# Kernel optimization log

Hardware: AMD Instinct MI355X
Metric: run time of the kernel (lower is better)

The kernel has to match this reference:

```python
import jax, jax.numpy as jnp
import numpy as np
from jax import lax

B, N = 4096, 512          # batch, sequence length (input_dim = 2*N)
H1, H2 = 64, 256          # hidden sizes of the two stacked LSTMs
E = 20                    # embed dim
OUT = 2


def _lstm_step(x, h, c, Wih, Whh, b):
    # gates in PyTorch order: i, f, g, o
    g = x @ Wih.T + h @ Whh.T + b
    i, f, gg, o = jnp.split(g, 4, axis=-1)
    c_new = jax.nn.sigmoid(f) * c + jax.nn.sigmoid(i) * jnp.tanh(gg)
    h_new = jax.nn.sigmoid(o) * jnp.tanh(c_new)
    return h_new, c_new


def setup_inputs() -> dict:
    key = jax.random.key(0)
    ks = jax.random.split(key, 9)
    s = lambda fan_in: 1.0 / np.sqrt(fan_in)
    return {
        "x": jax.random.normal(ks[0], (B, 2 * N), dtype=jnp.float32),
        "W_embed": jax.random.uniform(ks[1], (E, 2), minval=-s(2), maxval=s(2), dtype=jnp.float32),
        "Wih1": jax.random.uniform(ks[2], (4 * H1, E), minval=-s(H1), maxval=s(H1), dtype=jnp.float32),
        "Whh1": jax.random.uniform(ks[3], (4 * H1, H1), minval=-s(H1), maxval=s(H1), dtype=jnp.float32),
        "b1": jax.random.uniform(ks[4], (4 * H1,), minval=-s(H1), maxval=s(H1), dtype=jnp.float32),
        "Wih2": jax.random.uniform(ks[5], (4 * H2, H1), minval=-s(H2), maxval=s(H2), dtype=jnp.float32),
        "Whh2": jax.random.uniform(ks[6], (4 * H2, H2), minval=-s(H2), maxval=s(H2), dtype=jnp.float32),
        "b2": jax.random.uniform(ks[7], (4 * H2,), minval=-s(H2), maxval=s(H2), dtype=jnp.float32),
        "Wout": jax.random.uniform(ks[8], (OUT, H2), minval=-s(H2), maxval=s(H2), dtype=jnp.float32),
        "bout": jnp.zeros((OUT,), dtype=jnp.float32),
    }


def reference(x, W_embed, Wih1, Whh1, b1, Wih2, Whh2, b2, Wout, bout):
    b = x.shape[0]
    tokens = x.reshape(b, -1, 2).transpose(1, 0, 2)         # (n, b, 2)
    embedded = jax.nn.relu(tokens @ W_embed.T)              # (n, b, 20)

    def step(carry, xt):
        h, c = carry
        h, c = _lstm_step(xt, h, c, Wih1, Whh1, b1)
        return (h, c), None

    h0 = jnp.zeros((b, H1), dtype=x.dtype)
    (h64, _), _ = lax.scan(step, (h0, h0), embedded)        # last hidden (b, 64)

    # second LSTM applied to the 2-D last-hidden as a single timestep
    hz = jnp.zeros((b, H2), dtype=x.dtype)
    h256, _ = _lstm_step(h64, hz, hz, Wih2, Whh2, b2)       # (b, 256)

    return h256 @ Wout.T + bout                             # (b, 2)
```

## Files before the change

kernel.cpp:

```cpp
#include <hip/hip_runtime.h>

typedef _Float16 f16x8 __attribute__((ext_vector_type(8)));
typedef float    f32x4 __attribute__((ext_vector_type(4)));

#define NSTEP 512
#define CHUNK 8
#define NCHUNK (NSTEP / CHUNK)
#define LOG2E     1.4426950408889634f
#define TWOLOG2E  2.8853900817779268f

__device__ __forceinline__ float exp2_(float v) { return __builtin_amdgcn_exp2f(v); }

__device__ __forceinline__ float lstm_act_(float gi, float gf, float gg, float go, float& c) {
    float eg = exp2_(gg);
    float ei = exp2_(gi);
    float ef = exp2_(gf);
    float eo = exp2_(go);
    float X  = (eg + 1.0f) * (1.0f + ei);
    float Y  = 1.0f + ef;
    float r  = __builtin_amdgcn_rcpf(X * Y);
    c = fmaf(r * X, c, (eg - 1.0f) * (r * Y));
    float ec = exp2_(fminf(c * TWOLOG2E, 30.0f));
    float r2 = __builtin_amdgcn_rcpf((ec + 1.0f) * (1.0f + eo));
    return (ec - 1.0f) * r2;
}
__device__ __forceinline__ float sig_(float v) {
    return __builtin_amdgcn_rcpf(1.0f + exp2_(-v * LOG2E));
}
__device__ __forceinline__ float tanh_(float v) {
    return 1.0f - 2.0f * __builtin_amdgcn_rcpf(exp2_(v * TWOLOG2E) + 1.0f);
}

__global__ __launch_bounds__(1024, 1) void lstm_mfma16_kernel(
    const float* __restrict__ x,     const float* __restrict__ Wemb,
    const float* __restrict__ Wih1,  const float* __restrict__ Whh1,
    const float* __restrict__ b1,    const float* __restrict__ Wih2,
    const float* __restrict__ b2,    const float* __restrict__ Wout,
    const float* __restrict__ bout,  float* __restrict__ out)
{
    __shared__ __align__(16) _Float16 P[2][2][4][16][8];
    __shared__ __align__(16) _Float16 Pe[CHUNK][4][16][8];
    __shared__ __align__(16) float h2tmp[16 * 64];
    __shared__ __align__(16) float h2s[256 * 16];
    __shared__ float part[64 * 16 * 2];

    const int t   = threadIdx.x;
    const int l   = t & 63;
    const int tau = t >> 6;
    const int m   = l & 15;
    const int q   = l >> 4;
    const int b0  = blockIdx.x * 16;

    f16x8 whh[2], whE;
    {
        const int g = m & 3;
        const float sc = (g == 2) ? TWOLOG2E : -LOG2E;
        const int n = g * 64 + 4 * tau + (m >> 2);
        #pragma unroll
        for (int c = 0; c < 2; ++c) {
            #pragma unroll
            for (int jj = 0; jj < 8; ++jj)
                whh[c][jj] = (_Float16)(Whh1[n * 64 + c * 32 + (q << 3) + jj] * sc);
        }
        #pragma unroll
        for (int jj = 0; jj < 8; ++jj) {
            int k = (q << 3) + jj;
            whE[jj] = (_Float16)((k < 20) ? Wih1[n * 20 + k] * sc : 0.0f);
        }
    }
    f32x4 bias4;
    #pragma unroll
    for (int r = 0; r < 4; ++r) {
        float sc = (r == 2) ? TWOLOG2E : -LOG2E;
        bias4[r] = b1[r * 64 + 4 * tau + q] * sc;
    }

    const int myu = 4 * tau + q;
    _Float16* hw0 = &P[0][myu >> 5][(myu >> 3) & 3][m][myu & 7];

    const float* xp[3]; _Float16* pe[3];
    float we0[3], we1[3];
    bool val[3];
    float2 xv[3];
    #pragma unroll
    for (int k = 0; k < 3; ++k) {
        int v  = t + 1024 * k;
        val[k] = (v < CHUNK * 320);
        int vv = val[k] ? v : 0;
        int d  = vv % 20, pr = vv / 20;
        int bb = pr & 15, s = pr >> 4;
        we0[k] = Wemb[2 * d];
        we1[k] = Wemb[2 * d + 1];
        pe[k]  = &Pe[s][d >> 3][bb][d & 7];
        xp[k]  = x + (size_t)(b0 + bb) * (2 * NSTEP) + 2 * s;
        xv[k]  = *(const float2*)xp[k];
    }

    ((_Float16*)P)[t] = (_Float16)0.0f;
    {
        _Float16* pz = (_Float16*)Pe;
        #pragma unroll
        for (int k = 0; k < 4; ++k) pz[t + 1024 * k] = (_Float16)0.0f;
    }
    __syncthreads();

    float cst = 0.0f;
    for (int ch = 0; ch < NCHUNK; ++ch) {
        #pragma unroll
        for (int k = 0; k < 3; ++k)
            if (val[k])
                *pe[k] = (_Float16)fmaxf(fmaf(xv[k].x, we0[k], xv[k].y * we1[k]), 0.0f);
        if (ch + 1 < NCHUNK) {
            #pragma unroll
            for (int k = 0; k < 3; ++k) { xp[k] += 16; xv[k] = *(const float2*)xp[k]; }
        }
        __syncthreads();

        f32x4 ax[CHUNK];
        #pragma unroll
        for (int j = 0; j < CHUNK; ++j) {
            f16x8 fe = *(const f16x8*)&Pe[j][q][m][0];
            ax[j] = __builtin_amdgcn_mfma_f32_16x16x32_f16(whE, fe, bias4, 0, 0, 0);
        }

        #pragma unroll
        for (int j = 0; j < CHUNK; ++j) {
            const int pr = j & 1;
            f16x8 f0 = *(const f16x8*)&P[pr][0][q][m][0];
            f16x8 f1 = *(const f16x8*)&P[pr][1][q][m][0];
            f32x4 a = __builtin_amdgcn_mfma_f32_16x16x32_f16(whh[0], f0, ax[j], 0, 0, 0);
            a = __builtin_amdgcn_mfma_f32_16x16x32_f16(whh[1], f1, a, 0, 0, 0);
            float hv = lstm_act_(a[0], a[1], a[2], a[3], cst);
            hw0[(pr ^ 1) * 1024] = (_Float16)hv;
            __syncthreads();
        }
    }

    {
        int b = t >> 6, k = t & 63;
        h2tmp[t] = (float)P[0][k >> 5][(k >> 3) & 3][b][k & 7];
    }
    __syncthreads();

    {
        const int u = t & 255;
        const int bh0 = (t >> 8) * 4;
        float acci[4], accg[4], acco[4];
        float bi2 = b2[u], bg2 = b2[512 + u], bo2 = b2[768 + u];
        #pragma unroll
        for (int b = 0; b < 4; ++b) { acci[b] = bi2; accg[b] = bg2; acco[b] = bo2; }
        for (int k4 = 0; k4 < 64; k4 += 4) {
            float4 wi = *(const float4*)&Wih2[(size_t)u * 64 + k4];
            float4 wg = *(const float4*)&Wih2[(size_t)(512 + u) * 64 + k4];
            float4 wo = *(const float4*)&Wih2[(size_t)(768 + u) * 64 + k4];
            #pragma unroll
            for (int b = 0; b < 4; ++b) {
                float4 hb = *(const float4*)&h2tmp[(bh0 + b) * 64 + k4];
                acci[b] += wi.x * hb.x + wi.y * hb.y + wi.z * hb.z + wi.w * hb.w;
                accg[b] += wg.x * hb.x + wg.y * hb.y + wg.z * hb.z + wg.w * hb.w;
                acco[b] += wo.x * hb.x + wo.y * hb.y + wo.z * hb.z + wo.w * hb.w;
            }
        }
        #pragma unroll
        for (int b = 0; b < 4; ++b) {
            float c2 = sig_(acci[b]) * tanh_(accg[b]);
            h2s[u * 16 + bh0 + b] = sig_(acco[b]) * tanh_(c2);
        }
    }
    __syncthreads();

    {
        int b = t & 15, grp = t >> 4;
        float p0 = 0.f, p1 = 0.f;
        #pragma unroll
        for (int uu = grp * 4; uu < grp * 4 + 4; ++uu) {
            float hvv = h2s[uu * 16 + b];
            p0 += hvv * Wout[uu];
            p1 += hvv * Wout[256 + uu];
        }
        part[(grp * 16 + b) * 2 + 0] = p0;
        part[(grp * 16 + b) * 2 + 1] = p1;
    }
    __syncthreads();
    if (t < 32) {
        int b = t >> 1, o = t & 1;
        float s0 = bout[o];
        for (int grp = 0; grp < 64; ++grp) s0 += part[(grp * 16 + b) * 2 + o];
        out[(size_t)(b0 + b) * 2 + o] = s0;
    }
}

extern "C" void kernel_launch(void* const* d_in, const int* in_sizes, int n_in,
                              void* d_out, int out_size, void* d_ws, size_t ws_size,
                              hipStream_t stream) {
    const float* x    = (const float*)d_in[0];
    const float* Wemb = (const float*)d_in[1];
    const float* Wih1 = (const float*)d_in[2];
    const float* Whh1 = (const float*)d_in[3];
    const float* b1   = (const float*)d_in[4];
    const float* Wih2 = (const float*)d_in[5];
    const float* b2   = (const float*)d_in[7];
    const float* Wout = (const float*)d_in[8];
    const float* bout = (const float*)d_in[9];
    float* out = (float*)d_out;

    lstm_mfma16_kernel<<<256, 1024, 0, stream>>>(
        x, Wemb, Wih1, Whh1, b1, Wih2, b2, Wout, bout, out);
}
```

Baseline: 310.0 us.

## Halve block to 512 threads with two gate tiles per wave

Each block now runs 8 waves instead of 16, and each wave computes two 16-row gate tiles (units A and B) per timestep, reusing the same loaded h fragments for both. This halves the number of waves taking part in the per-step __syncthreads barrier, which dominates the 512-step serial recurrence. It also adds ILP by interleaving two independent MFMA chains and activation sequences. The cost is more registers per thread and a longer per-wave critical path per step. Launch bounds allow two blocks per CU, but the grid is still 256 blocks.

```diff
diff --git a/kernel.cpp b/kernel.cpp
--- a/kernel.cpp
+++ b/kernel.cpp
@@ -31,7 +31,7 @@
     return 1.0f - 2.0f * __builtin_amdgcn_rcpf(exp2_(v * TWOLOG2E) + 1.0f);
 }
 
-__global__ __launch_bounds__(1024, 1) void lstm_mfma16_kernel(
+__global__ __launch_bounds__(512, 2) void lstm_mfma16_kernel(
     const float* __restrict__ x,     const float* __restrict__ Wemb,
     const float* __restrict__ Wih1,  const float* __restrict__ Whh1,
     const float* __restrict__ b1,    const float* __restrict__ Wih2,
@@ -42,52 +42,53 @@
     __shared__ __align__(16) _Float16 Pe[CHUNK][4][16][8];
     __shared__ __align__(16) float h2tmp[16 * 64];
     __shared__ __align__(16) float h2s[256 * 16];
-    __shared__ float part[64 * 16 * 2];
+    __shared__ float part[32 * 16 * 2];
 
     const int t   = threadIdx.x;
     const int l   = t & 63;
-    const int tau = t >> 6;
+    const int w   = t >> 6;
     const int m   = l & 15;
     const int q   = l >> 4;
     const int b0  = blockIdx.x * 16;
 
-    f16x8 whh[2], whE;
-    {
+    f16x8 whh[2][2], whE[2];
+    f32x4 bias4[2];
+    #pragma unroll
+    for (int tt = 0; tt < 2; ++tt) {
+        const int tau = 2 * w + tt;
         const int g = m & 3;
         const float sc = (g == 2) ? TWOLOG2E : -LOG2E;
         const int n = g * 64 + 4 * tau + (m >> 2);
         #pragma unroll
-        for (int c = 0; c < 2; ++c) {
+        for (int c = 0; c < 2; ++c)
             #pragma unroll
             for (int jj = 0; jj < 8; ++jj)
-                whh[c][jj] = (_Float16)(Whh1[n * 64 + c * 32 + (q << 3) + jj] * sc);
-        }
+                whh[tt][c][jj] = (_Float16)(Whh1[n * 64 + c * 32 + (q << 3) + jj] * sc);
         #pragma unroll
         for (int jj = 0; jj < 8; ++jj) {
             int k = (q << 3) + jj;
-            whE[jj] = (_Float16)((k < 20) ? Wih1[n * 20 + k] * sc : 0.0f);
-        }
-    }
-    f32x4 bias4;
+            whE[tt][jj] = (_Float16)((k < 20) ? Wih1[n * 20 + k] * sc : 0.0f);
+        }
+        #pragma unroll
+        for (int r = 0; r < 4; ++r) {
+            float scr = (r == 2) ? TWOLOG2E : -LOG2E;
+            bias4[tt][r] = b1[r * 64 + 4 * tau + q] * scr;
+        }
+    }
+
+    const int myuA = 8 * w + q;
+    const int myuB = 8 * w + 4 + q;
+    _Float16* hwA = &P[0][myuA >> 5][(myuA >> 3) & 3][m][myuA & 7];
+    _Float16* hwB = &P[0][myuB >> 5][(myuB >> 3) & 3][m][myuB & 7];
+    const _Float16* rb = &P[0][0][q][m][0];
+
+    const float* xp[5]; _Float16* pe[5];
+    float we0[5], we1[5];
+    float2 xv[5];
     #pragma unroll
-    for (int r = 0; r < 4; ++r) {
-        float sc = (r == 2) ? TWOLOG2E : -LOG2E;
-        bias4[r] = b1[r * 64 + 4 * tau + q] * sc;
-    }
-
-    const int myu = 4 * tau + q;
-    _Float16* hw0 = &P[0][myu >> 5][(myu >> 3) & 3][m][myu & 7];
-
-    const float* xp[3]; _Float16* pe[3];
-    float we0[3], we1[3];
-    bool val[3];
-    float2 xv[3];
-    #pragma unroll
-    for (int k = 0; k < 3; ++k) {
-        int v  = t + 1024 * k;
-        val[k] = (v < CHUNK * 320);
-        int vv = val[k] ? v : 0;
-        int d  = vv % 20, pr = vv / 20;
+    for (int k = 0; k < 5; ++k) {
+        int v  = t + 512 * k;
+        int d  = v % 20, pr = v / 20;
         int bb = pr & 15, s = pr >> 4;
         we0[k] = Wemb[2 * d];
         we1[k] = Wemb[2 * d + 1];
@@ -96,65 +97,72 @@
         xv[k]  = *(const float2*)xp[k];
     }
 
-    ((_Float16*)P)[t] = (_Float16)0.0f;
+    ((_Float16*)P)[t]       = (_Float16)0.0f;
+    ((_Float16*)P)[t + 512] = (_Float16)0.0f;
     {
         _Float16* pz = (_Float16*)Pe;
         #pragma unroll
-        for (int k = 0; k < 4; ++k) pz[t + 1024 * k] = (_Float16)0.0f;
-    }
-    __syncthreads();
-
-    float cst = 0.0f;
+        for (int k = 0; k < 8; ++k) pz[t + 512 * k] = (_Float16)0.0f;
+    }
+    __syncthreads();
+
+    float cA = 0.0f, cB = 0.0f;
     for (int ch = 0; ch < NCHUNK; ++ch) {
         #pragma unroll
-        for (int k = 0; k < 3; ++k)
-            if (val[k])
-                *pe[k] = (_Float16)fmaxf(fmaf(xv[k].x, we0[k], xv[k].y * we1[k]), 0.0f);
+        for (int k = 0; k < 5; ++k)
+            *pe[k] = (_Float16)fmaxf(fmaf(xv[k].x, we0[k], xv[k].y * we1[k]), 0.0f);
         if (ch + 1 < NCHUNK) {
             #pragma unroll
-            for (int k = 0; k < 3; ++k) { xp[k] += 16; xv[k] = *(const float2*)xp[k]; }
+            for (int k = 0; k < 5; ++k) { xp[k] += 16; xv[k] = *(const float2*)xp[k]; }
         }
         __syncthreads();
 
-        f32x4 ax[CHUNK];
+        f32x4 axA[CHUNK], axB[CHUNK];
         #pragma unroll
         for (int j = 0; j < CHUNK; ++j) {
             f16x8 fe = *(const f16x8*)&Pe[j][q][m][0];
-            ax[j] = __builtin_amdgcn_mfma_f32_16x16x32_f16(whE, fe, bias4, 0, 0, 0);
+            axA[j] = __builtin_amdgcn_mfma_f32_16x16x32_f16(whE[0], fe, bias4[0], 0, 0, 0);
+            axB[j] = __builtin_amdgcn_mfma_f32_16x16x32_f16(whE[1], fe, bias4[1], 0, 0, 0);
         }
 
         #pragma unroll
         for (int j = 0; j < CHUNK; ++j) {
             const int pr = j & 1;
-            f16x8 f0 = *(const f16x8*)&P[pr][0][q][m][0];
-            f16x8 f1 = *(const f16x8*)&P[pr][1][q][m][0];
-            f32x4 a = __builtin_amdgcn_mfma_f32_16x16x32_f16(whh[0], f0, ax[j], 0, 0, 0);
-            a = __builtin_amdgcn_mfma_f32_16x16x32_f16(whh[1], f1, a, 0, 0, 0);
-            float hv = lstm_act_(a[0], a[1], a[2], a[3], cst);
-            hw0[(pr ^ 1) * 1024] = (_Float16)hv;
+            f16x8 f0 = *(const f16x8*)(rb + pr * 1024);
+            f16x8 f1 = *(const f16x8*)(rb + pr * 1024 + 512);
+            f32x4 aA = __builtin_amdgcn_mfma_f32_16x16x32_f16(whh[0][0], f0, axA[j], 0, 0, 0);
+            f32x4 aB = __builtin_amdgcn_mfma_f32_16x16x32_f16(whh[1][0], f0, axB[j], 0, 0, 0);
+            aA = __builtin_amdgcn_mfma_f32_16x16x32_f16(whh[0][1], f1, aA, 0, 0, 0);
+            aB = __builtin_amdgcn_mfma_f32_16x16x32_f16(whh[1][1], f1, aB, 0, 0, 0);
+            float hA = lstm_act_(aA[0], aA[1], aA[2], aA[3], cA);
+            float hB = lstm_act_(aB[0], aB[1], aB[2], aB[3], cB);
+            hwA[(pr ^ 1) * 1024] = (_Float16)hA;
+            hwB[(pr ^ 1) * 1024] = (_Float16)hB;
             __syncthreads();
         }
     }
 
-    {
-        int b = t >> 6, k = t & 63;
-        h2tmp[t] = (float)P[0][k >> 5][(k >> 3) & 3][b][k & 7];
+    #pragma unroll
+    for (int r = 0; r < 2; ++r) {
+        int tt = t + 512 * r;
+        int b = tt >> 6, k = tt & 63;
+        h2tmp[tt] = (float)P[0][k >> 5][(k >> 3) & 3][b][k & 7];
     }
     __syncthreads();
 
     {
         const int u = t & 255;
-        const int bh0 = (t >> 8) * 4;
-        float acci[4], accg[4], acco[4];
+        const int bh0 = (t >> 8) * 8;
+        float acci[8], accg[8], acco[8];
         float bi2 = b2[u], bg2 = b2[512 + u], bo2 = b2[768 + u];
         #pragma unroll
-        for (int b = 0; b < 4; ++b) { acci[b] = bi2; accg[b] = bg2; acco[b] = bo2; }
+        for (int b = 0; b < 8; ++b) { acci[b] = bi2; accg[b] = bg2; acco[b] = bo2; }
         for (int k4 = 0; k4 < 64; k4 += 4) {
             float4 wi = *(const float4*)&Wih2[(size_t)u * 64 + k4];
             float4 wg = *(const float4*)&Wih2[(size_t)(512 + u) * 64 + k4];
             float4 wo = *(const float4*)&Wih2[(size_t)(768 + u) * 64 + k4];
             #pragma unroll
-            for (int b = 0; b < 4; ++b) {
+            for (int b = 0; b < 8; ++b) {
                 float4 hb = *(const float4*)&h2tmp[(bh0 + b) * 64 + k4];
                 acci[b] += wi.x * hb.x + wi.y * hb.y + wi.z * hb.z + wi.w * hb.w;
                 accg[b] += wg.x * hb.x + wg.y * hb.y + wg.z * hb.z + wg.w * hb.w;
@@ -162,7 +170,7 @@
             }
         }
         #pragma unroll
-        for (int b = 0; b < 4; ++b) {
+        for (int b = 0; b < 8; ++b) {
             float c2 = sig_(acci[b]) * tanh_(accg[b]);
             h2s[u * 16 + bh0 + b] = sig_(acco[b]) * tanh_(c2);
         }
@@ -173,7 +181,7 @@
         int b = t & 15, grp = t >> 4;
         float p0 = 0.f, p1 = 0.f;
         #pragma unroll
-        for (int uu = grp * 4; uu < grp * 4 + 4; ++uu) {
+        for (int uu = grp * 8; uu < grp * 8 + 8; ++uu) {
             float hvv = h2s[uu * 16 + b];
             p0 += hvv * Wout[uu];
             p1 += hvv * Wout[256 + uu];
@@ -185,7 +193,7 @@
     if (t < 32) {
         int b = t >> 1, o = t & 1;
         float s0 = bout[o];
-        for (int grp = 0; grp < 64; ++grp) s0 += part[(grp * 16 + b) * 2 + o];
+        for (int grp = 0; grp < 32; ++grp) s0 += part[(grp * 16 + b) * 2 + o];
         out[(size_t)(b0 + b) * 2 + o] = s0;
     }
 }
@@ -204,6 +212,6 @@
     const float* bout = (const float*)d_in[9];
     float* out = (float*)d_out;
 
-    lstm_mfma16_kernel<<<256, 1024, 0, stream>>>(
+    lstm_mfma16_kernel<<<256, 512, 0, stream>>>(
         x, Wemb, Wih1, Whh1, b1, Wih2, b2, Wout, bout, out);
 }
```

Result: faster. 297.1 us (-4.2%).
